# Kernel optimization log

Measured on AMD Instinct MI355X. Metric: run time of the kernel, lower is better.

Reference implementation:

```python
import jax, jax.numpy as jnp
import numpy as np

B, S, D = 4, 4096, 2048
NUM_MODALITIES = 2


def setup_inputs() -> dict:
    key = jax.random.key(0)
    k_x, k_t, k_w0, k_b0, k_w1, k_b1 = jax.random.split(key, 6)
    scale = 1.0 / np.sqrt(D)
    return {
        "hidden_states": jax.random.normal(k_x, (B, S, D), dtype=jnp.float32),
        "type_ids": jax.random.randint(k_t, (B, S), 0, NUM_MODALITIES, dtype=jnp.int32),
        "W0": jax.random.uniform(k_w0, (D, D), jnp.float32, -scale, scale),
        "b0": jax.random.uniform(k_b0, (D,), jnp.float32, -scale, scale),
        "W1": jax.random.uniform(k_w1, (D, D), jnp.float32, -scale, scale),
        "b1": jax.random.uniform(k_b1, (D,), jnp.float32, -scale, scale),
    }


def reference(hidden_states, type_ids, W0, b0, W1, b1):
    # Original: gather tokens where type_ids == i, apply expert i's Linear,
    # scatter into a zero-init [B, S, out_dim] buffer. The masks partition
    # all tokens, so this equals a masked mixture of the two dense GEMMs.
    y0 = jnp.einsum("bsd,ed->bse", hidden_states, W0) + b0  # expert 0
    y1 = jnp.einsum("bsd,ed->bse", hidden_states, W1) + b1  # expert 1
    m0 = (type_ids == 0)[..., None]
    m1 = (type_ids == 1)[..., None]
    zero = jnp.zeros((), dtype=y0.dtype)
    return jnp.where(m0, y0, zero) + jnp.where(m1, y1, zero)
```

## Files before the change

kernel.cpp:

```cpp
#include <hip/hip_runtime.h>
#include <hip/hip_bf16.h>
#include <stdint.h>


#define T_TOK 16384
#define DDIM  2048
#define NT_K  32
#define MT    64
#define NTILE 8

typedef __attribute__((ext_vector_type(4))) float          f32x4;
typedef __attribute__((ext_vector_type(8))) short          bf16x8;
typedef __attribute__((ext_vector_type(2))) unsigned int   u32x2;

#define WS_HBF   0ull
#define WS_W0BF  67108864ull
#define WS_W1BF  75497472ull
#define WS_META  83886080ull
#define WS_IDX   83886208ull
#define WS_NEED  (WS_IDX + 65536ull)

__device__ __forceinline__ unsigned short cvt1_bf16(float f) {
  unsigned u = __builtin_bit_cast(unsigned, f);
  unsigned rnd = 0x7fffu + ((u >> 16) & 1u);
  return (unsigned short)((u + rnd) >> 16);
}

__device__ __forceinline__ void gload_lds16(const void* g, void* l) {
  __builtin_amdgcn_global_load_lds(
      (const __attribute__((address_space(1))) unsigned int*)g,
      (__attribute__((address_space(3))) unsigned int*)l, 16, 0, 0);
}

#define BAR()     asm volatile("s_barrier" ::: "memory")
#define VMCNT10() asm volatile("s_waitcnt vmcnt(10)" ::: "memory")
#define VMCNT0()  asm volatile("s_waitcnt vmcnt(0)" ::: "memory")
#define LGKM0()   asm volatile("s_waitcnt lgkmcnt(0)" ::: "memory")

__global__ void k_prep(const float* __restrict__ H, const float* __restrict__ W0,
                       const float* __restrict__ W1, const int* __restrict__ typ,
                       unsigned short* __restrict__ Hbf,
                       unsigned short* __restrict__ W0bf,
                       unsigned short* __restrict__ W1bf,
                       int* __restrict__ meta) {
  const int gid = blockIdx.x * blockDim.x + threadIdx.x;
  if (gid < T_TOK && typ[gid] == 0) atomicAdd(&meta[0], 1);
  const int nH = T_TOK * DDIM / 4;
  const int nW = DDIM * DDIM / 4;
  const int total = nH + 2 * nW;
  const int stride = gridDim.x * blockDim.x;
  for (int i = gid; i < total; i += stride) {
    const float* s; unsigned short* d; int j;
    if (i < nH)           { s = H;  d = Hbf;  j = i; }
    else if (i < nH + nW) { s = W0; d = W0bf; j = i - nH; }
    else                  { s = W1; d = W1bf; j = i - nH - nW; }
    f32x4 v = ((const f32x4*)s)[j];
    unsigned p0 = (unsigned)cvt1_bf16(v[0]) | ((unsigned)cvt1_bf16(v[1]) << 16);
    unsigned p1 = (unsigned)cvt1_bf16(v[2]) | ((unsigned)cvt1_bf16(v[3]) << 16);
    u32x2 o; o[0] = p0; o[1] = p1;
    ((u32x2*)d)[j] = o;
  }
}

__global__ void k_scatter(const int* __restrict__ typ, int* __restrict__ meta,
                          int* __restrict__ idx) {
  int i = blockIdx.x * blockDim.x + threadIdx.x;
  if (i >= T_TOK) return;
  int c0 = meta[0];
  int t = typ[i];
  int pos = (t == 0) ? atomicAdd(&meta[2], 1) : c0 + atomicAdd(&meta[3], 1);
  idx[pos] = i;
}

__global__ __launch_bounds__(512, 2) void k_gemm256(
    const unsigned short* __restrict__ Hbf,
    const unsigned short* __restrict__ W0bf,
    const unsigned short* __restrict__ W1bf,
    const float* __restrict__ B0, const float* __restrict__ B1,
    const int* __restrict__ meta, const int* __restrict__ idx,
    float* __restrict__ OUT)
{
  __shared__ char lds[131072];

  const int orig = blockIdx.x;
  const int wg = (orig & 7) * 64 + (orig >> 3);
  int my = wg >> 3;
  const int bx = wg & 7;

  const int c0 = meta[0];
  int ms = c0 >> 8; if (ms > MT - 1) ms = MT - 1;
  my = (my == 0) ? ms : (my == ms) ? 0 : my;

  const int tid  = threadIdx.x;
  const int lane = tid & 63;
  const int wid  = tid >> 6;
  const int wr   = wid >> 2;
  const int wc   = wid & 3;
  const int fr   = lane & 15;
  const int g    = lane >> 4;

  const int start = my * 256;
  const int e0    = (start >= c0) ? 1 : 0;
  const int e1    = (start < c0 && c0 < start + 256) ? 1 : e0;
  const int colBase = bx * 256;

  const int cs = (lane & 3) ^ ((lane >> 3) & 3);
  const char* aS[2];
  int rt[2];
#pragma unroll
  for (int l = 0; l < 2; ++l) {
    int ch = 2 * wid + l;
    rt[l] = ch * 16 + (lane >> 2);
    int orow = idx[start + rt[l]];
    aS[l] = (const char*)Hbf + (size_t)orow * 4096 + cs * 16;
  }
  const int chB = (2 * wid) * 1024;

  const int sw = (g ^ ((fr >> 1) & 3)) << 4;
  int aF[8], bF[4];
#pragma unroll
  for (int m = 0; m < 8; ++m) aF[m] = ((wr * 128 + m * 16 + fr) << 6) + sw;
#pragma unroll
  for (int n = 0; n < 4; ++n) bF[n] = ((wc * 64 + n * 16 + fr) << 6) + sw;

  for (int e = e0; e <= e1; ++e) {
    const unsigned short* Wb = e ? W1bf : W0bf;
    const char* wS[2];
#pragma unroll
    for (int l = 0; l < 2; ++l)
      wS[l] = (const char*)(Wb + (size_t)(colBase + rt[l]) * DDIM) + cs * 16;

    f32x4 acc[8][4];
#pragma unroll
    for (int m = 0; m < 8; ++m)
#pragma unroll
      for (int n = 0; n < 4; ++n) acc[m][n] = (f32x4)0.0f;

    auto STAGE_A = [&](int d, int kh, int tn) {
      char* dst = lds + (d << 15) + (kh << 14) + chB;
      int ko = tn * 128 + kh * 64;
      gload_lds16(aS[0] + ko, dst);
      gload_lds16(aS[1] + ko, dst + 1024);
    };
    auto STAGE_B = [&](int d, int kh, int tn) {
      char* dst = lds + 65536 + (d << 15) + (kh << 14) + chB;
      int ko = tn * 128 + kh * 64;
      gload_lds16(wS[0] + ko, dst);
      gload_lds16(wS[1] + ko, dst + 1024);
    };

    VMCNT0();
    BAR();

    STAGE_B(0, 0, 0); STAGE_A(0, 0, 0);
    STAGE_B(0, 1, 0); STAGE_A(0, 1, 0);
    STAGE_B(1, 0, 1); STAGE_A(1, 0, 1);
    STAGE_B(1, 1, 1);
    VMCNT10();
    BAR();

#pragma unroll 2
    for (int t = 0; t < NT_K; ++t) {
      const int c = t & 1, d = c ^ 1;
      int t1 = t + 1; if (t1 >= NT_K) t1 = NT_K - 1;
      int t2 = t + 2; if (t2 >= NT_K) t2 = NT_K - 1;
      const char* Ak0 = lds + (c << 15);
      const char* Ak1 = Ak0 + 16384;
      const char* Bk0 = lds + 65536 + (c << 15);
      const char* Bk1 = Bk0 + 16384;

      bf16x8 a[4], b[4];

#pragma unroll
      for (int m = 0; m < 4; ++m) a[m] = *(const bf16x8*)(Ak0 + aF[m]);
#pragma unroll
      for (int n = 0; n < 4; ++n) b[n] = *(const bf16x8*)(Bk0 + bF[n]);
      STAGE_A(d, 1, t1);
      BAR(); LGKM0();
      __builtin_amdgcn_s_setprio(1);
#pragma unroll
      for (int n = 0; n < 4; ++n)
#pragma unroll
        for (int m = 0; m < 4; ++m)
          acc[m][n] = __builtin_amdgcn_mfma_f32_16x16x32_bf16(a[m], b[n], acc[m][n], 0, 0, 0);
      __builtin_amdgcn_s_setprio(0);
      BAR();

#pragma unroll
      for (int m = 0; m < 4; ++m) a[m] = *(const bf16x8*)(Ak0 + aF[m + 4]);
      STAGE_B(c, 0, t2);
      VMCNT10();
      BAR(); LGKM0();
      __builtin_amdgcn_s_setprio(1);
#pragma unroll
      for (int n = 0; n < 4; ++n)
#pragma unroll
        for (int m = 0; m < 4; ++m)
          acc[m + 4][n] = __builtin_amdgcn_mfma_f32_16x16x32_bf16(a[m], b[n], acc[m + 4][n], 0, 0, 0);
      __builtin_amdgcn_s_setprio(0);
      BAR();

#pragma unroll
      for (int m = 0; m < 4; ++m) a[m] = *(const bf16x8*)(Ak1 + aF[m]);
#pragma unroll
      for (int n = 0; n < 4; ++n) b[n] = *(const bf16x8*)(Bk1 + bF[n]);
      STAGE_A(c, 0, t2);
      BAR(); LGKM0();
      __builtin_amdgcn_s_setprio(1);
#pragma unroll
      for (int n = 0; n < 4; ++n)
#pragma unroll
        for (int m = 0; m < 4; ++m)
          acc[m][n] = __builtin_amdgcn_mfma_f32_16x16x32_bf16(a[m], b[n], acc[m][n], 0, 0, 0);
      __builtin_amdgcn_s_setprio(0);
      BAR();

#pragma unroll
      for (int m = 0; m < 4; ++m) a[m] = *(const bf16x8*)(Ak1 + aF[m + 4]);
      STAGE_B(c, 1, t2);
      VMCNT10();
      BAR(); LGKM0();
      __builtin_amdgcn_s_setprio(1);
#pragma unroll
      for (int n = 0; n < 4; ++n)
#pragma unroll
        for (int m = 0; m < 4; ++m)
          acc[m + 4][n] = __builtin_amdgcn_mfma_f32_16x16x32_bf16(a[m], b[n], acc[m + 4][n], 0, 0, 0);
      __builtin_amdgcn_s_setprio(0);
      BAR();
    }

    const float* Bv = e ? B1 : B0;
    float bias[4];
    int cols[4];
#pragma unroll
    for (int n = 0; n < 4; ++n) {
      cols[n] = colBase + wc * 64 + n * 16 + fr;
      bias[n] = Bv[cols[n]];
    }
#pragma unroll
    for (int m = 0; m < 8; ++m) {
      int lb = wr * 128 + m * 16 + (g << 2);
#pragma unroll
      for (int j = 0; j < 4; ++j) {
        int p = start + lb + j;
        if (((p >= c0) ? 1 : 0) != e) continue;
        int orow = idx[p];
        float* op = OUT + (size_t)orow * DDIM;
#pragma unroll
        for (int n = 0; n < 4; ++n) op[cols[n]] = acc[m][n][j] + bias[n];
      }
    }
  }
}

#define BMd 64
#define BNd 64
#define BKd 32
#define LDW 36

__device__ __forceinline__ bf16x8 cvt_bf16x8(f32x4 lo, f32x4 hi) {
  bf16x8 r;
#pragma unroll
  for (int i = 0; i < 4; ++i) {
    r[i]     = (short)cvt1_bf16(lo[i]);
    r[i + 4] = (short)cvt1_bf16(hi[i]);
  }
  return r;
}

__global__ __launch_bounds__(256, 2) void mot_mfma_diag(
    const float* __restrict__ H,  const int* __restrict__ TYP,
    const float* __restrict__ W0, const float* __restrict__ B0,
    const float* __restrict__ W1, const float* __restrict__ B1,
    float* __restrict__ OUT)
{
  __shared__ float As[BMd * LDW];
  __shared__ float W0s[BNd * LDW];
  __shared__ float W1s[BNd * LDW];

  const int tid = threadIdx.x;
  const int rowBase = blockIdx.y * BMd;
  const int colBase = blockIdx.x * BNd;
  const int srow  = tid >> 3;
  const int scol4 = (tid & 7) << 2;
  const float* hA  = H  + (size_t)(rowBase + srow) * DDIM + scol4;
  const float* hW0 = W0 + (size_t)(colBase + srow) * DDIM + scol4;
  const float* hW1 = W1 + (size_t)(colBase + srow) * DDIM + scol4;

  const int lane = tid & 63;
  const int w    = tid >> 6;
  const int fr   = lane & 15;
  const int g    = lane >> 4;

  f32x4 acc0[4], acc1[4];
#pragma unroll
  for (int m = 0; m < 4; ++m) { acc0[m] = (f32x4)0.0f; acc1[m] = (f32x4)0.0f; }

  for (int k0 = 0; k0 < DDIM; k0 += BKd) {
    f32x4 va[2], v0[2], v1[2];
#pragma unroll
    for (int p = 0; p < 2; ++p) {
      va[p] = *(const f32x4*)(hA  + (size_t)p * 32 * DDIM);
      v0[p] = *(const f32x4*)(hW0 + (size_t)p * 32 * DDIM);
      v1[p] = *(const f32x4*)(hW1 + (size_t)p * 32 * DDIM);
    }
    hA += BKd; hW0 += BKd; hW1 += BKd;
    __syncthreads();
#pragma unroll
    for (int p = 0; p < 2; ++p) {
      int r = srow + 32 * p;
      *(f32x4*)(&As [r * LDW + scol4]) = va[p];
      *(f32x4*)(&W0s[r * LDW + scol4]) = v0[p];
      *(f32x4*)(&W1s[r * LDW + scol4]) = v1[p];
    }
    __syncthreads();

    bf16x8 af[4];
#pragma unroll
    for (int m = 0; m < 4; ++m) {
      const float* ap = &As[(m * 16 + fr) * LDW + g * 8];
      af[m] = cvt_bf16x8(*(const f32x4*)ap, *(const f32x4*)(ap + 4));
    }
    const float* b0p = &W0s[(w * 16 + fr) * LDW + g * 8];
    const float* b1p = &W1s[(w * 16 + fr) * LDW + g * 8];
    bf16x8 bf0 = cvt_bf16x8(*(const f32x4*)b0p, *(const f32x4*)(b0p + 4));
    bf16x8 bf1 = cvt_bf16x8(*(const f32x4*)b1p, *(const f32x4*)(b1p + 4));
#pragma unroll
    for (int m = 0; m < 4; ++m) {
      acc0[m] = __builtin_amdgcn_mfma_f32_16x16x32_bf16(af[m], bf0, acc0[m], 0, 0, 0);
      acc1[m] = __builtin_amdgcn_mfma_f32_16x16x32_bf16(af[m], bf1, acc1[m], 0, 0, 0);
    }
  }

  const int col = colBase + w * 16 + fr;
  const float bz0 = B0[col];
  const float bz1 = B1[col];
#pragma unroll
  for (int m = 0; m < 4; ++m)
#pragma unroll
    for (int j = 0; j < 4; ++j) {
      int row = rowBase + m * 16 + (g << 2) + j;
      int t = TYP[row];
      OUT[(size_t)row * DDIM + col] = (t == 0) ? (acc0[m][j] + bz0) : (acc1[m][j] + bz1);
    }
}

extern "C" void kernel_launch(void* const* d_in, const int* in_sizes, int n_in,
                              void* d_out, int out_size, void* d_ws, size_t ws_size,
                              hipStream_t stream) {
  const float* H   = (const float*)d_in[0];
  const int*   TYP = (const int*)  d_in[1];
  const float* W0  = (const float*)d_in[2];
  const float* B0v = (const float*)d_in[3];
  const float* W1  = (const float*)d_in[4];
  const float* B1v = (const float*)d_in[5];
  float* OUT = (float*)d_out;

  if (ws_size < WS_NEED) {
    dim3 grid(DDIM / BNd, T_TOK / BMd);
    mot_mfma_diag<<<grid, dim3(256), 0, stream>>>(H, TYP, W0, B0v, W1, B1v, OUT);
    return;
  }

  unsigned short* Hbf  = (unsigned short*)((char*)d_ws + WS_HBF);
  unsigned short* W0bf = (unsigned short*)((char*)d_ws + WS_W0BF);
  unsigned short* W1bf = (unsigned short*)((char*)d_ws + WS_W1BF);
  int* meta = (int*)((char*)d_ws + WS_META);
  int* idx  = (int*)((char*)d_ws + WS_IDX);

  hipMemsetAsync(meta, 0, 16, stream);
  k_prep   <<<4096, 256, 0, stream>>>(H, W0, W1, TYP, Hbf, W0bf, W1bf, meta);
  k_scatter<<<64,   256, 0, stream>>>(TYP, meta, idx);
  k_gemm256<<<MT * NTILE, 512, 0, stream>>>(Hbf, W0bf, W1bf, B0v, B1v, meta, idx, OUT);
}
```

Baseline: 238.0 us.

## Restructure GEMM main loop to prefetch LDS fragments during MFMA phases

The K-loop pipeline changes from a two-tile-ahead global prefetch with vmcnt(10) waits to a one-tile-ahead scheme. LDS fragment reads for the next MFMA phase are issued before the current phase's MFMAs run, using extra register buffers (a2, b2, an) and sched_barrier fences. The aim is to hide LDS read latency behind matrix work and drop the LGKM wait that used to sit right before each MFMA block. In exchange the prefetch distance for global loads is shorter, the kernel uses more registers, and the buffer-reuse ordering now depends on barrier placement.

```diff
diff --git a/kernel.cpp b/kernel.cpp
--- a/kernel.cpp
+++ b/kernel.cpp
@@ -33,9 +33,11 @@
 }
 
 #define BAR()     asm volatile("s_barrier" ::: "memory")
-#define VMCNT10() asm volatile("s_waitcnt vmcnt(10)" ::: "memory")
+#define VMCNT2()  asm volatile("s_waitcnt vmcnt(2)" ::: "memory")
+#define VMCNT4()  asm volatile("s_waitcnt vmcnt(4)" ::: "memory")
 #define VMCNT0()  asm volatile("s_waitcnt vmcnt(0)" ::: "memory")
 #define LGKM0()   asm volatile("s_waitcnt lgkmcnt(0)" ::: "memory")
+#define SCHEDBAR() __builtin_amdgcn_sched_barrier(0)
 
 __global__ void k_prep(const float* __restrict__ H, const float* __restrict__ W0,
                        const float* __restrict__ W1, const int* __restrict__ typ,
@@ -152,31 +154,30 @@
     VMCNT0();
     BAR();
 
-    STAGE_B(0, 0, 0); STAGE_A(0, 0, 0);
-    STAGE_B(0, 1, 0); STAGE_A(0, 1, 0);
-    STAGE_B(1, 0, 1); STAGE_A(1, 0, 1);
-    STAGE_B(1, 1, 1);
-    VMCNT10();
+    STAGE_A(0, 0, 0); STAGE_B(0, 0, 0); STAGE_A(0, 1, 0); STAGE_B(0, 1, 0);
+    VMCNT4();
     BAR();
+
+    bf16x8 a[4], b[4], a2[4], b2[4], an[4];
+#pragma unroll
+    for (int m = 0; m < 4; ++m) a[m] = *(const bf16x8*)(lds + aF[m]);
+#pragma unroll
+    for (int n = 0; n < 4; ++n) b[n] = *(const bf16x8*)(lds + 65536 + bF[n]);
+    LGKM0(); SCHEDBAR();
 
 #pragma unroll 2
     for (int t = 0; t < NT_K; ++t) {
       const int c = t & 1, d = c ^ 1;
-      int t1 = t + 1; if (t1 >= NT_K) t1 = NT_K - 1;
-      int t2 = t + 2; if (t2 >= NT_K) t2 = NT_K - 1;
+      int t1 = t + 1; if (t1 == NT_K) t1 = NT_K - 1;
       const char* Ak0 = lds + (c << 15);
       const char* Ak1 = Ak0 + 16384;
-      const char* Bk0 = lds + 65536 + (c << 15);
-      const char* Bk1 = Bk0 + 16384;
-
-      bf16x8 a[4], b[4];
-
-#pragma unroll
-      for (int m = 0; m < 4; ++m) a[m] = *(const bf16x8*)(Ak0 + aF[m]);
-#pragma unroll
-      for (int n = 0; n < 4; ++n) b[n] = *(const bf16x8*)(Bk0 + bF[n]);
-      STAGE_A(d, 1, t1);
-      BAR(); LGKM0();
+      const char* Bk1 = lds + 65536 + (c << 15) + 16384;
+      const char* Ad0 = lds + (d << 15);
+      const char* Bd0 = lds + 65536 + (d << 15);
+
+      STAGE_A(d, 0, t1);
+#pragma unroll
+      for (int m = 0; m < 4; ++m) an[m] = *(const bf16x8*)(Ak0 + aF[m + 4]);
       __builtin_amdgcn_s_setprio(1);
 #pragma unroll
       for (int n = 0; n < 4; ++n)
@@ -184,51 +185,56 @@
         for (int m = 0; m < 4; ++m)
           acc[m][n] = __builtin_amdgcn_mfma_f32_16x16x32_bf16(a[m], b[n], acc[m][n], 0, 0, 0);
       __builtin_amdgcn_s_setprio(0);
+      VMCNT2();
+      LGKM0(); SCHEDBAR();
       BAR();
 
-#pragma unroll
-      for (int m = 0; m < 4; ++m) a[m] = *(const bf16x8*)(Ak0 + aF[m + 4]);
-      STAGE_B(c, 0, t2);
-      VMCNT10();
-      BAR(); LGKM0();
+      STAGE_B(d, 0, t1);
+#pragma unroll
+      for (int m = 0; m < 4; ++m) a2[m] = *(const bf16x8*)(Ak1 + aF[m]);
+#pragma unroll
+      for (int n = 0; n < 4; ++n) b2[n] = *(const bf16x8*)(Bk1 + bF[n]);
       __builtin_amdgcn_s_setprio(1);
 #pragma unroll
       for (int n = 0; n < 4; ++n)
 #pragma unroll
         for (int m = 0; m < 4; ++m)
-          acc[m + 4][n] = __builtin_amdgcn_mfma_f32_16x16x32_bf16(a[m], b[n], acc[m + 4][n], 0, 0, 0);
+          acc[m + 4][n] = __builtin_amdgcn_mfma_f32_16x16x32_bf16(an[m], b[n], acc[m + 4][n], 0, 0, 0);
       __builtin_amdgcn_s_setprio(0);
+      LGKM0(); SCHEDBAR();
       BAR();
 
-#pragma unroll
-      for (int m = 0; m < 4; ++m) a[m] = *(const bf16x8*)(Ak1 + aF[m]);
-#pragma unroll
-      for (int n = 0; n < 4; ++n) b[n] = *(const bf16x8*)(Bk1 + bF[n]);
-      STAGE_A(c, 0, t2);
-      BAR(); LGKM0();
+      STAGE_A(d, 1, t1);
+#pragma unroll
+      for (int m = 0; m < 4; ++m) an[m] = *(const bf16x8*)(Ak1 + aF[m + 4]);
       __builtin_amdgcn_s_setprio(1);
 #pragma unroll
       for (int n = 0; n < 4; ++n)
 #pragma unroll
         for (int m = 0; m < 4; ++m)
-          acc[m][n] = __builtin_amdgcn_mfma_f32_16x16x32_bf16(a[m], b[n], acc[m][n], 0, 0, 0);
+          acc[m][n] = __builtin_amdgcn_mfma_f32_16x16x32_bf16(a2[m], b2[n], acc[m][n], 0, 0, 0);
       __builtin_amdgcn_s_setprio(0);
+      VMCNT2();
+      LGKM0(); SCHEDBAR();
       BAR();
 
-#pragma unroll
-      for (int m = 0; m < 4; ++m) a[m] = *(const bf16x8*)(Ak1 + aF[m + 4]);
-      STAGE_B(c, 1, t2);
-      VMCNT10();
-      BAR(); LGKM0();
+      STAGE_B(d, 1, t1);
+#pragma unroll
+      for (int m = 0; m < 4; ++m) a[m] = *(const bf16x8*)(Ad0 + aF[m]);
+#pragma unroll
+      for (int n = 0; n < 4; ++n) b[n] = *(const bf16x8*)(Bd0 + bF[n]);
       __builtin_amdgcn_s_setprio(1);
 #pragma unroll
       for (int n = 0; n < 4; ++n)
 #pragma unroll
         for (int m = 0; m < 4; ++m)
-          acc[m + 4][n] = __builtin_amdgcn_mfma_f32_16x16x32_bf16(a[m], b[n], acc[m + 4][n], 0, 0, 0);
+          acc[m + 4][n] = __builtin_amdgcn_mfma_f32_16x16x32_bf16(an[m], b2[n], acc[m + 4][n], 0, 0, 0);
       __builtin_amdgcn_s_setprio(0);
+      LGKM0(); SCHEDBAR();
       BAR();
     }
+
+    VMCNT0();
 
     const float* Bv = e ? B1 : B0;
     float bias[4];
```

After: 261.3 us. 9.8% more time.
